# Kernel optimization log

Measured on AMD Instinct MI355X. Metric: run time of the kernel, lower is better.

Reference implementation:

```python
import jax, jax.numpy as jnp
import numpy as np

B, S, D, H = 2, 2048, 1024, 16
HEAD_DIM = D // H
SCALE = HEAD_DIM ** -0.5


def setup_inputs() -> dict:
    key = jax.random.key(0)
    k1, k2, k3 = jax.random.split(key, 3)
    x = jax.random.normal(k1, (B, S, D), dtype=jnp.float32)
    # torch nn.Linear convention: weight is [out_features, in_features], y = x @ W.T + b
    W_qkv = jax.random.normal(k2, (3 * D, D), dtype=jnp.float32) * 0.02  # qkv Linear, bias=False
    W_out = jax.random.normal(k3, (D, D), dtype=jnp.float32) * 0.02
    b_out = jnp.zeros((D,), dtype=jnp.float32)
    return {"x": x, "W_qkv": W_qkv, "W_out": W_out, "b_out": b_out}


def reference(x, W_qkv, W_out, b_out):
    b, s, d_model = x.shape
    # qkv projection (no bias), then split 'b c (qkv h d) -> qkv b h c d'
    qkv = (x @ W_qkv.T).reshape(b, s, 3, H, HEAD_DIM).transpose(2, 0, 3, 1, 4)
    q, k, v = qkv[0], qkv[1], qkv[2]  # each [b, h, s, hd]
    # naive full attention: scores materialized as [b, h, s, s]
    attn = jax.nn.softmax(jnp.einsum('bhxd,bhyd->bhxy', q, k) * SCALE, axis=-1)
    # dropout is identity (rate 0 / eval mode)
    o = jnp.einsum('bhxy,bhyd->bhxd', attn, v)
    o = o.transpose(0, 2, 1, 3).reshape(b, s, d_model)  # 'b h c d -> b c (h d)'
    return o @ W_out.T + b_out
```

## Files before the change

### kernel.cpp

```cpp
#include <hip/hip_runtime.h>


typedef __attribute__((ext_vector_type(8))) short short8;
typedef __attribute__((ext_vector_type(4))) float f32x4;
typedef unsigned short ushort_t;
typedef unsigned int uint32;

#define AS1 __attribute__((address_space(1)))
#define AS3 __attribute__((address_space(3)))

__device__ __forceinline__ void gload_lds16(const void* gp, void* lp) {
    __builtin_amdgcn_global_load_lds((const AS1 void*)gp, (AS3 void*)lp, 16, 0, 0);
}

#if __has_builtin(__builtin_amdgcn_exp2f)
#define EXP2F(x) __builtin_amdgcn_exp2f(x)
#else
#define EXP2F(x) exp2f(x)
#endif

__device__ __forceinline__ uint32 rhu(float f) { return __float_as_uint(f) + 0x8000u; }
#if __has_builtin(__builtin_amdgcn_perm)
__device__ __forceinline__ uint32 pk2bf(float a, float b) {
    return __builtin_amdgcn_perm(rhu(b), rhu(a), 0x07060302u);
}
#else
__device__ __forceinline__ uint32 pk2bf(float a, float b) {
    return (rhu(a) >> 16) | (rhu(b) & 0xffff0000u);
}
#endif
__device__ __forceinline__ ushort_t f2bf(float f) { return (ushort_t)(rhu(f) >> 16); }

__global__ void cvt_all(const float* __restrict__ x, ushort_t* __restrict__ xb,
                        const float* __restrict__ wq, ushort_t* __restrict__ wqb,
                        const float* __restrict__ wo, ushort_t* __restrict__ wob) {
    int blk = blockIdx.x;
    const float* in; ushort_t* out;
    if (blk < 4096)      { in = x;  out = xb;  }
    else if (blk < 7168) { in = wq; out = wqb; blk -= 4096; }
    else                 { in = wo; out = wob; blk -= 7168; }
    const int i = (blk * 256 + threadIdx.x) * 4;
    const float4 v = *(const float4*)(in + i);
    uint2 pk;
    pk.x = pk2bf(v.x, v.y);
    pk.y = pk2bf(v.z, v.w);
    *(uint2*)(out + i) = pk;
}

__global__ __launch_bounds__(256, 2)
void gemm_qkv(const ushort_t* __restrict__ A, const ushort_t* __restrict__ B,
              ushort_t* __restrict__ Cb, ushort_t* __restrict__ vT,
              int M, int N, int K, int ldc, float qScale) {
    __shared__ ushort_t lA[2][128 * 32];
    __shared__ ushort_t lB[2][128 * 32];
    const int tid = threadIdx.x;
    const int wave = tid >> 6, lane = tid & 63;
    const int quad = lane >> 4, l16 = lane & 15;
    const int wr = wave >> 1, wc = wave & 1;
    const int mBase = blockIdx.y * 128, nBase = blockIdx.x * 128;

    f32x4 acc[4][4];
#pragma unroll
    for (int i = 0; i < 4; i++)
#pragma unroll
        for (int j = 0; j < 4; j++) acc[i][j] = (f32x4){0.f, 0.f, 0.f, 0.f};

    const int ar = tid >> 2;
    const int ac = (((tid & 3) ^ ((ar >> 1) & 3)) * 8);
    const int rsw = ((l16 >> 1) & 3);

    const ushort_t* aptr = A + (size_t)(mBase + ar) * K + ac;
    const ushort_t* bptr = B + (size_t)(nBase + ar) * K + ac;

#define G1_STAGE(buf, k0)                                                            \
    {                                                                                \
        _Pragma("unroll") for (int c = 0; c < 2; c++) {                              \
            gload_lds16(aptr + (size_t)(c * 64) * K + (k0), lA[buf] + c * 2048 + wave * 512); \
            gload_lds16(bptr + (size_t)(c * 64) * K + (k0), lB[buf] + c * 2048 + wave * 512); \
        }                                                                            \
    }

    G1_STAGE(0, 0);
    for (int k0 = 0; k0 < K; k0 += 32) {
        const int cur = (k0 >> 5) & 1;
        __syncthreads();
        if (k0 + 32 < K) G1_STAGE(cur ^ 1, k0 + 32);

        short8 af[4], bf[4];
#pragma unroll
        for (int i = 0; i < 4; i++)
            af[i] = *(const short8*)(lA[cur] + (wr * 64 + i * 16 + l16) * 32 + ((quad ^ rsw) * 8));
#pragma unroll
        for (int j = 0; j < 4; j++)
            bf[j] = *(const short8*)(lB[cur] + (wc * 64 + j * 16 + l16) * 32 + ((quad ^ rsw) * 8));
#pragma unroll
        for (int i = 0; i < 4; i++)
#pragma unroll
            for (int j = 0; j < 4; j++)
                acc[i][j] = __builtin_amdgcn_mfma_f32_16x16x32_bf16(af[i], bf[j], acc[i][j], 0, 0, 0);
    }

    if (nBase >= 2048) {
#pragma unroll
        for (int i = 0; i < 4; i++)
#pragma unroll
            for (int j = 0; j < 4; j++) {
                const int row0 = mBase + wr * 64 + i * 16 + quad * 4;
                const int col = nBase + wc * 64 + j * 16 + l16 - 2048;
                const int b = row0 >> 11, s0 = row0 & 2047;
                uint2 pk;
                pk.x = pk2bf(acc[i][j][0], acc[i][j][1]);
                pk.y = pk2bf(acc[i][j][2], acc[i][j][3]);
                *(uint2*)(vT + ((size_t)(b * 16) * 64 + col) * 2048 + s0) = pk;
            }
        return;
    }
    const float cs = (nBase < 1024) ? qScale : 1.0f;
#pragma unroll
    for (int i = 0; i < 4; i++)
#pragma unroll
        for (int j = 0; j < 4; j++)
#pragma unroll
            for (int r = 0; r < 4; r++) {
                const int row = mBase + wr * 64 + i * 16 + quad * 4 + r;
                const int col = nBase + wc * 64 + j * 16 + l16;
                Cb[(size_t)row * ldc + col] = f2bf(acc[i][j][r] * cs);
            }
}

__global__ __launch_bounds__(256, 2)
void gemm_out(const ushort_t* __restrict__ A, const ushort_t* __restrict__ B,
              float* __restrict__ Cf, const float* __restrict__ bias,
              int M, int N, int K) {
    __shared__ ushort_t lA[2][64 * 64];
    __shared__ ushort_t lB[2][128 * 64];
    const int tid = threadIdx.x;
    const int wave = tid >> 6, lane = tid & 63;
    const int quad = lane >> 4, l16 = lane & 15;
    const int mBase = blockIdx.y * 64, nBase = blockIdx.x * 128;

    f32x4 acc[4][2];
#pragma unroll
    for (int i = 0; i < 4; i++)
#pragma unroll
        for (int j = 0; j < 2; j++) acc[i][j] = (f32x4){0.f, 0.f, 0.f, 0.f};

    const int sr = tid >> 3;
    const int sc = ((tid & 7) ^ (sr & 7)) * 8;
    const int swz = l16 & 7;

    const ushort_t* aptr = A + (size_t)(mBase + sr) * K + sc;
    const ushort_t* bptr = B + (size_t)(nBase + sr) * K + sc;

#define G2_STAGE(buf, k0)                                                              \
    {                                                                                  \
        _Pragma("unroll") for (int c = 0; c < 2; c++)                                  \
            gload_lds16(aptr + (size_t)(c * 32) * K + (k0), lA[buf] + c * 2048 + wave * 512); \
        _Pragma("unroll") for (int c = 0; c < 4; c++)                                  \
            gload_lds16(bptr + (size_t)(c * 32) * K + (k0), lB[buf] + c * 2048 + wave * 512); \
    }

    G2_STAGE(0, 0);
    for (int k0 = 0; k0 < K; k0 += 64) {
        const int cur = (k0 >> 6) & 1;
        __syncthreads();
        if (k0 + 64 < K) G2_STAGE(cur ^ 1, k0 + 64);

#pragma unroll
        for (int ks = 0; ks < 2; ks++) {
            short8 af[4], bf[2];
#pragma unroll
            for (int i = 0; i < 4; i++)
                af[i] = *(const short8*)(lA[cur] + (i * 16 + l16) * 64 + (((ks * 4 + quad) ^ swz) * 8));
#pragma unroll
            for (int j = 0; j < 2; j++)
                bf[j] = *(const short8*)(lB[cur] + (wave * 32 + j * 16 + l16) * 64 + (((ks * 4 + quad) ^ swz) * 8));
#pragma unroll
            for (int i = 0; i < 4; i++)
#pragma unroll
                for (int j = 0; j < 2; j++)
                    acc[i][j] = __builtin_amdgcn_mfma_f32_16x16x32_bf16(af[i], bf[j], acc[i][j], 0, 0, 0);
        }
    }

#pragma unroll
    for (int i = 0; i < 4; i++)
#pragma unroll
        for (int j = 0; j < 2; j++)
#pragma unroll
            for (int r = 0; r < 4; r++) {
                const int row = mBase + i * 16 + quad * 4 + r;
                const int col = nBase + wave * 32 + j * 16 + l16;
                Cf[(size_t)row * N + col] = acc[i][j][r] + bias[col];
            }
}

__global__ __launch_bounds__(256, 4)
void attn_flash(const ushort_t* __restrict__ qk, const ushort_t* __restrict__ vT,
                ushort_t* __restrict__ o) {
    __shared__ ushort_t lK[2][64 * 64];
    __shared__ ushort_t lV[2][64 * 64];
    __shared__ ushort_t lP[4][16 * 40];

    const int tid = threadIdx.x;
    const int wave = tid >> 6, lane = tid & 63;
    const int quad = lane >> 4, l16 = lane & 15;
    const int bh = blockIdx.y;
    const int b = bh >> 4, h = bh & 15;
    const size_t rowBase = (size_t)b * 2048;
    const int qCol = h * 64, kCol = 1024 + h * 64;
    const int qRow0 = blockIdx.x * 64;
    const int swz = l16 & 7;

    const int sr = tid >> 3;
    const int sc = ((tid & 7) ^ (sr & 7)) * 8;

#pragma unroll
    for (int cc = 0; cc < 2; cc++)
        gload_lds16(qk + (rowBase + qRow0 + cc * 32 + sr) * 2048 + qCol + sc,
                    lK[0] + cc * 2048 + wave * 512);
    __syncthreads();
    short8 qf[2];
#pragma unroll
    for (int ks = 0; ks < 2; ks++)
        qf[ks] = *(const short8*)(lK[0] + (wave * 16 + l16) * 64 + (((ks * 4 + quad) ^ swz) * 8));
    __syncthreads();

    short8 onesA;
#pragma unroll
    for (int i = 0; i < 8; i++) onesA[i] = (short)0x3F80;

    f32x4 oacc[4];
    f32x4 lacc = (f32x4){0.f, 0.f, 0.f, 0.f};
#pragma unroll
    for (int dt = 0; dt < 4; dt++) oacc[dt] = (f32x4){0.f, 0.f, 0.f, 0.f};

    const ushort_t* kptr = qk + (rowBase + sr) * 2048 + kCol + sc;
    const ushort_t* vptr = vT + ((size_t)bh * 64 + sr) * 2048 + sc;

#define AT_STAGE(buf, kt)                                                                 \
    {                                                                                     \
        _Pragma("unroll") for (int cc = 0; cc < 2; cc++)                                  \
            gload_lds16(kptr + (size_t)((kt) * 64 + cc * 32) * 2048, lK[buf] + cc * 2048 + wave * 512); \
        _Pragma("unroll") for (int cc = 0; cc < 2; cc++)                                  \
            gload_lds16(vptr + (size_t)(cc * 32) * 2048 + (kt) * 64, lV[buf] + cc * 2048 + wave * 512); \
    }

    AT_STAGE(0, 0);
    for (int kt = 0; kt < 32; kt++) {
        const int cur = kt & 1;
        __syncthreads();
        if (kt < 31) AT_STAGE(cur ^ 1, kt + 1);

        f32x4 sacc[4];
#pragma unroll
        for (int mt = 0; mt < 4; mt++) {
            const short8 k0 = *(const short8*)(lK[cur] + (mt * 16 + l16) * 64 + ((quad ^ swz) * 8));
            const short8 k1 = *(const short8*)(lK[cur] + (mt * 16 + l16) * 64 + (((4 + quad) ^ swz) * 8));
            f32x4 t = (f32x4){0.f, 0.f, 0.f, 0.f};
            t = __builtin_amdgcn_mfma_f32_16x16x32_bf16(k0, qf[0], t, 0, 0, 0);
            t = __builtin_amdgcn_mfma_f32_16x16x32_bf16(k1, qf[1], t, 0, 0, 0);
            sacc[mt] = t;
        }

#pragma unroll
        for (int kk = 0; kk < 2; kk++) {
#pragma unroll
            for (int t16 = 0; t16 < 2; t16++) {
                const f32x4 s = sacc[2 * kk + t16];
                uint2 pk;
                pk.x = pk2bf(EXP2F(s[0]), EXP2F(s[1]));
                pk.y = pk2bf(EXP2F(s[2]), EXP2F(s[3]));
                *(uint2*)(&lP[wave][l16 * 40 + t16 * 16 + quad * 4]) = pk;
            }
            const short8 pf = *(const short8*)(&lP[wave][l16 * 40 + quad * 8]);
            lacc = __builtin_amdgcn_mfma_f32_16x16x32_bf16(onesA, pf, lacc, 0, 0, 0);
#pragma unroll
            for (int dt = 0; dt < 4; dt++) {
                const short8 vf = *(const short8*)(lV[cur] + (dt * 16 + l16) * 64 +
                                                   (((kk * 4 + quad) ^ swz) * 8));
                oacc[dt] = __builtin_amdgcn_mfma_f32_16x16x32_bf16(vf, pf, oacc[dt], 0, 0, 0);
            }
        }
    }

    const float inv = 1.0f / lacc[0];
    const size_t row = rowBase + qRow0 + wave * 16 + l16;
#pragma unroll
    for (int dt = 0; dt < 4; dt++) {
        uint2 pk;
        pk.x = pk2bf(oacc[dt][0] * inv, oacc[dt][1] * inv);
        pk.y = pk2bf(oacc[dt][2] * inv, oacc[dt][3] * inv);
        *(uint2*)(o + row * 1024 + h * 64 + dt * 16 + quad * 4) = pk;
    }
}

extern "C" void kernel_launch(void* const* d_in, const int* in_sizes, int n_in,
                              void* d_out, int out_size, void* d_ws, size_t ws_size,
                              hipStream_t stream) {
    const float* x    = (const float*)d_in[0];
    const float* Wqkv = (const float*)d_in[1];
    const float* Wout = (const float*)d_in[2];
    const float* bout = (const float*)d_in[3];
    float* out = (float*)d_out;

    ushort_t* xb    = (ushort_t*)d_ws;
    ushort_t* wqkvb = xb + (size_t)4096 * 1024;
    ushort_t* woutb = wqkvb + (size_t)3072 * 1024;
    ushort_t* qkb   = woutb + (size_t)1024 * 1024;
    ushort_t* vTb   = qkb + (size_t)4096 * 2048;
    ushort_t* ob    = xb;

    const float SC = 0.125f * 1.44269504089f;

    cvt_all<<<8192, 256, 0, stream>>>(x, xb, Wqkv, wqkvb, Wout, woutb);
    gemm_qkv<<<dim3(24, 32), 256, 0, stream>>>(xb, wqkvb, qkb, vTb, 4096, 3072, 1024, 2048, SC);
    attn_flash<<<dim3(32, 32), 256, 0, stream>>>(qkb, vTb, ob);
    gemm_out<<<dim3(8, 64), 256, 0, stream>>>(ob, woutb, out, bout, 4096, 1024, 1024);
}
```

Baseline: 186.6 us.

## Split attention KV tile across wave groups with 128-row query blocks

The attention kernel now uses 512-thread blocks covering 128 query rows. Each wave handles 32 query rows and half of each 64-key tile, so every K/V fragment loaded from LDS feeds two query tiles. Partial output and row-sum accumulators from the two key halves are combined through shared memory at the end. This raises fragment reuse and halves K/V global traffic per query row, at the cost of half as many blocks, a final reduction pass, and more registers per wave.

```diff
diff --git a/kernel.cpp b/kernel.cpp
--- a/kernel.cpp
+++ b/kernel.cpp
@@ -195,55 +195,63 @@
             }
 }
 
-__global__ __launch_bounds__(256, 4)
+__global__ __launch_bounds__(512, 4)
 void attn_flash(const ushort_t* __restrict__ qk, const ushort_t* __restrict__ vT,
                 ushort_t* __restrict__ o) {
-    __shared__ ushort_t lK[2][64 * 64];
-    __shared__ ushort_t lV[2][64 * 64];
-    __shared__ ushort_t lP[4][16 * 40];
+    __shared__ ushort_t smem[26624];
 
     const int tid = threadIdx.x;
     const int wave = tid >> 6, lane = tid & 63;
     const int quad = lane >> 4, l16 = lane & 15;
-    const int bh = blockIdx.y;
-    const int b = bh >> 4, h = bh & 15;
+    const int qg = wave & 3, kg = wave >> 2;
+    const int bh = blockIdx.y, b = bh >> 4, h = bh & 15;
     const size_t rowBase = (size_t)b * 2048;
     const int qCol = h * 64, kCol = 1024 + h * 64;
-    const int qRow0 = blockIdx.x * 64;
+    const int qRow0 = blockIdx.x * 128;
     const int swz = l16 & 7;
 
+    ushort_t* lP = smem + 16384 + wave * 1280;
+
+    {
+        const int sr_ = tid >> 3;
+        const int sc_ = ((tid & 7) ^ (sr_ & 7)) * 8;
+#pragma unroll
+        for (int cc = 0; cc < 2; cc++)
+            gload_lds16(qk + (rowBase + qRow0 + cc * 64 + sr_) * 2048 + qCol + sc_,
+                        smem + 16384 + cc * 4096 + wave * 512);
+    }
+    __syncthreads();
+    short8 qf[2][2];
+#pragma unroll
+    for (int qt = 0; qt < 2; qt++)
+#pragma unroll
+        for (int ks = 0; ks < 2; ks++)
+            qf[qt][ks] = *(const short8*)(smem + 16384 + (qg * 32 + qt * 16 + l16) * 64 +
+                                          (((ks * 4 + quad) ^ swz) * 8));
+    __syncthreads();
+
+    short8 onesA;
+#pragma unroll
+    for (int i = 0; i < 8; i++) onesA[i] = (short)0x3F80;
+
+    f32x4 oacc[4][2];
+    f32x4 lacc[2];
+#pragma unroll
+    for (int qt = 0; qt < 2; qt++) {
+        lacc[qt] = (f32x4){0.f, 0.f, 0.f, 0.f};
+#pragma unroll
+        for (int dt = 0; dt < 4; dt++) oacc[dt][qt] = (f32x4){0.f, 0.f, 0.f, 0.f};
+    }
+
     const int sr = tid >> 3;
-    const int sc = ((tid & 7) ^ (sr & 7)) * 8;
-
-#pragma unroll
-    for (int cc = 0; cc < 2; cc++)
-        gload_lds16(qk + (rowBase + qRow0 + cc * 32 + sr) * 2048 + qCol + sc,
-                    lK[0] + cc * 2048 + wave * 512);
-    __syncthreads();
-    short8 qf[2];
-#pragma unroll
-    for (int ks = 0; ks < 2; ks++)
-        qf[ks] = *(const short8*)(lK[0] + (wave * 16 + l16) * 64 + (((ks * 4 + quad) ^ swz) * 8));
-    __syncthreads();
-
-    short8 onesA;
-#pragma unroll
-    for (int i = 0; i < 8; i++) onesA[i] = (short)0x3F80;
-
-    f32x4 oacc[4];
-    f32x4 lacc = (f32x4){0.f, 0.f, 0.f, 0.f};
-#pragma unroll
-    for (int dt = 0; dt < 4; dt++) oacc[dt] = (f32x4){0.f, 0.f, 0.f, 0.f};
-
-    const ushort_t* kptr = qk + (rowBase + sr) * 2048 + kCol + sc;
-    const ushort_t* vptr = vT + ((size_t)bh * 64 + sr) * 2048 + sc;
-
-#define AT_STAGE(buf, kt)                                                                 \
-    {                                                                                     \
-        _Pragma("unroll") for (int cc = 0; cc < 2; cc++)                                  \
-            gload_lds16(kptr + (size_t)((kt) * 64 + cc * 32) * 2048, lK[buf] + cc * 2048 + wave * 512); \
-        _Pragma("unroll") for (int cc = 0; cc < 2; cc++)                                  \
-            gload_lds16(vptr + (size_t)(cc * 32) * 2048 + (kt) * 64, lV[buf] + cc * 2048 + wave * 512); \
+    const int sch = ((tid & 7) ^ (sr & 7)) * 8;
+    const ushort_t* kptr = qk + (rowBase + sr) * 2048 + kCol + sch;
+    const ushort_t* vptr = vT + ((size_t)bh * 64 + sr) * 2048 + sch;
+
+#define AT_STAGE(buf, kt)                                                            \
+    {                                                                                \
+        gload_lds16(kptr + (size_t)(kt) * 64 * 2048, smem + (buf) * 4096 + wave * 512); \
+        gload_lds16(vptr + (kt) * 64, smem + 8192 + (buf) * 4096 + wave * 512);      \
     }
 
     AT_STAGE(0, 0);
@@ -251,47 +259,82 @@
         const int cur = kt & 1;
         __syncthreads();
         if (kt < 31) AT_STAGE(cur ^ 1, kt + 1);
-
-        f32x4 sacc[4];
-#pragma unroll
-        for (int mt = 0; mt < 4; mt++) {
-            const short8 k0 = *(const short8*)(lK[cur] + (mt * 16 + l16) * 64 + ((quad ^ swz) * 8));
-            const short8 k1 = *(const short8*)(lK[cur] + (mt * 16 + l16) * 64 + (((4 + quad) ^ swz) * 8));
-            f32x4 t = (f32x4){0.f, 0.f, 0.f, 0.f};
-            t = __builtin_amdgcn_mfma_f32_16x16x32_bf16(k0, qf[0], t, 0, 0, 0);
-            t = __builtin_amdgcn_mfma_f32_16x16x32_bf16(k1, qf[1], t, 0, 0, 0);
-            sacc[mt] = t;
-        }
-
-#pragma unroll
-        for (int kk = 0; kk < 2; kk++) {
-#pragma unroll
-            for (int t16 = 0; t16 < 2; t16++) {
-                const f32x4 s = sacc[2 * kk + t16];
+        const ushort_t* lK = smem + cur * 4096;
+        const ushort_t* lV = smem + 8192 + cur * 4096;
+
+        f32x4 sacc[2][2];
+#pragma unroll
+        for (int mh = 0; mh < 2; mh++) {
+            const int krow = kg * 32 + mh * 16 + l16;
+            const short8 k0 = *(const short8*)(lK + krow * 64 + ((quad ^ swz) * 8));
+            const short8 k1 = *(const short8*)(lK + krow * 64 + (((4 + quad) ^ swz) * 8));
+#pragma unroll
+            for (int qt = 0; qt < 2; qt++) {
+                f32x4 t = (f32x4){0.f, 0.f, 0.f, 0.f};
+                t = __builtin_amdgcn_mfma_f32_16x16x32_bf16(k0, qf[qt][0], t, 0, 0, 0);
+                t = __builtin_amdgcn_mfma_f32_16x16x32_bf16(k1, qf[qt][1], t, 0, 0, 0);
+                sacc[mh][qt] = t;
+            }
+        }
+
+#pragma unroll
+        for (int qt = 0; qt < 2; qt++)
+#pragma unroll
+            for (int mh = 0; mh < 2; mh++) {
+                const f32x4 s = sacc[mh][qt];
                 uint2 pk;
                 pk.x = pk2bf(EXP2F(s[0]), EXP2F(s[1]));
                 pk.y = pk2bf(EXP2F(s[2]), EXP2F(s[3]));
-                *(uint2*)(&lP[wave][l16 * 40 + t16 * 16 + quad * 4]) = pk;
-            }
-            const short8 pf = *(const short8*)(&lP[wave][l16 * 40 + quad * 8]);
-            lacc = __builtin_amdgcn_mfma_f32_16x16x32_bf16(onesA, pf, lacc, 0, 0, 0);
+                *(uint2*)(&lP[(qt * 16 + l16) * 40 + mh * 16 + quad * 4]) = pk;
+            }
+
+        short8 pf[2];
+#pragma unroll
+        for (int qt = 0; qt < 2; qt++) {
+            pf[qt] = *(const short8*)(&lP[(qt * 16 + l16) * 40 + quad * 8]);
+            lacc[qt] = __builtin_amdgcn_mfma_f32_16x16x32_bf16(onesA, pf[qt], lacc[qt], 0, 0, 0);
+        }
+#pragma unroll
+        for (int dt = 0; dt < 4; dt++) {
+            const short8 vf = *(const short8*)(lV + (dt * 16 + l16) * 64 +
+                                               (((kg * 4 + quad) ^ swz) * 8));
+#pragma unroll
+            for (int qt = 0; qt < 2; qt++)
+                oacc[dt][qt] = __builtin_amdgcn_mfma_f32_16x16x32_bf16(vf, pf[qt], oacc[dt][qt], 0, 0, 0);
+        }
+    }
+
+    __syncthreads();
+    float* red = (float*)smem;
+    if (kg == 1) {
+#pragma unroll
+        for (int qt = 0; qt < 2; qt++) {
+            if (quad == 0) red[8192 + qg * 32 + qt * 16 + l16] = lacc[qt][0];
+#pragma unroll
+            for (int dt = 0; dt < 4; dt++)
+                *(f32x4*)(red + (((qg * 4 + dt) * 2 + qt) * 64 + lane) * 4) = oacc[dt][qt];
+        }
+    }
+    __syncthreads();
+    if (kg == 0) {
+        float linv[2];
+#pragma unroll
+        for (int qt = 0; qt < 2; qt++)
+            linv[qt] = 1.0f / (lacc[qt][0] + red[8192 + qg * 32 + qt * 16 + l16]);
+#pragma unroll
+        for (int qt = 0; qt < 2; qt++) {
+            const size_t row = rowBase + qRow0 + qg * 32 + qt * 16 + l16;
 #pragma unroll
             for (int dt = 0; dt < 4; dt++) {
-                const short8 vf = *(const short8*)(lV[cur] + (dt * 16 + l16) * 64 +
-                                                   (((kk * 4 + quad) ^ swz) * 8));
-                oacc[dt] = __builtin_amdgcn_mfma_f32_16x16x32_bf16(vf, pf, oacc[dt], 0, 0, 0);
-            }
-        }
-    }
-
-    const float inv = 1.0f / lacc[0];
-    const size_t row = rowBase + qRow0 + wave * 16 + l16;
-#pragma unroll
-    for (int dt = 0; dt < 4; dt++) {
-        uint2 pk;
-        pk.x = pk2bf(oacc[dt][0] * inv, oacc[dt][1] * inv);
-        pk.y = pk2bf(oacc[dt][2] * inv, oacc[dt][3] * inv);
-        *(uint2*)(o + row * 1024 + h * 64 + dt * 16 + quad * 4) = pk;
+                const f32x4 r = *(const f32x4*)(red + (((qg * 4 + dt) * 2 + qt) * 64 + lane) * 4);
+                uint2 pk;
+                pk.x = pk2bf((oacc[dt][qt][0] + r[0]) * linv[qt],
+                             (oacc[dt][qt][1] + r[1]) * linv[qt]);
+                pk.y = pk2bf((oacc[dt][qt][2] + r[2]) * linv[qt],
+                             (oacc[dt][qt][3] + r[3]) * linv[qt]);
+                *(uint2*)(o + row * 1024 + h * 64 + dt * 16 + quad * 4) = pk;
+            }
+        }
     }
 }
 
@@ -315,6 +358,6 @@
 
     cvt_all<<<8192, 256, 0, stream>>>(x, xb, Wqkv, wqkvb, Wout, woutb);
     gemm_qkv<<<dim3(24, 32), 256, 0, stream>>>(xb, wqkvb, qkb, vTb, 4096, 3072, 1024, 2048, SC);
-    attn_flash<<<dim3(32, 32), 256, 0, stream>>>(qkb, vTb, ob);
+    attn_flash<<<dim3(16, 32), 512, 0, stream>>>(qkb, vTb, ob);
     gemm_out<<<dim3(8, 64), 256, 0, stream>>>(ob, woutb, out, bout, 4096, 1024, 1024);
 }
```

Result: faster. 181.4 us (-2.8%).
